# Optimization experiments

Hardware: AMD Instinct MI355X
Metric: run time of the kernel (lower is better)

The kernel has to match this reference:

```python
import jax, jax.numpy as jnp
import numpy as np


def _gcn_layer(x, W, b, src, dst, norm, n_nodes):
    # PyG GCNConv: h = x @ W, then degree-normalized scatter-add over edges (incl. self loops), then + bias
    h = x @ W                                   # [N, F_out]
    msg = h[src] * norm[:, None]                # [E+N, F_out]
    out = jax.ops.segment_sum(msg, dst, num_segments=n_nodes)
    return out + b


def _norm_and_loops(edge_index, n_nodes):
    # add self loops, compute symmetric normalization deg^-1/2[src]*deg^-1/2[dst]
    loop = jnp.arange(n_nodes, dtype=edge_index.dtype)
    src = jnp.concatenate([edge_index[0], loop])
    dst = jnp.concatenate([edge_index[1], loop])
    deg = jax.ops.segment_sum(jnp.ones_like(dst, dtype=jnp.float32), dst, num_segments=n_nodes)
    dinv = jnp.where(deg > 0, jax.lax.rsqrt(deg), 0.0)
    norm = dinv[src] * dinv[dst]
    return src, dst, norm


def setup_inputs() -> dict:
    key = jax.random.key(0)
    k1, k2, k3, k4 = jax.random.split(key, 4)
    N, E, F = 100000, 1600000, 512
    x = jax.random.normal(k1, (N, F), dtype=jnp.float32)
    edge_index = jax.random.randint(k2, (2, E), 0, N, dtype=jnp.int64)
    W1 = jax.random.normal(k3, (F, 128), dtype=jnp.float32) * (1.0 / np.sqrt(F))
    b1 = jnp.zeros((128,), dtype=jnp.float32)
    W2 = jax.random.normal(k4, (128, 64), dtype=jnp.float32) * (1.0 / np.sqrt(128))
    b2 = jnp.zeros((64,), dtype=jnp.float32)
    return {"x": x, "edge_index": edge_index, "W1": W1, "b1": b1, "W2": W2, "b2": b2}


def reference(x, edge_index, W1, b1, W2, b2):
    n_nodes = x.shape[0]
    src, dst, norm = _norm_and_loops(edge_index, n_nodes)
    h = jax.nn.relu(_gcn_layer(x, W1, b1, src, dst, norm, n_nodes))
    z = jax.nn.relu(_gcn_layer(h, W2, b2, src, dst, norm, n_nodes))
    return z
```

## Files before the change

### kernel.cpp

```cpp
#include <hip/hip_runtime.h>

#define SCAN_B 1024

using f16x8 = __attribute__((ext_vector_type(8))) _Float16;
using f32x4 = __attribute__((ext_vector_type(4))) float;
typedef _Float16 half4v __attribute__((ext_vector_type(4)));
typedef _Float16 half8v __attribute__((ext_vector_type(8)));


__global__ void zero2_kernel(int* __restrict__ a, int* __restrict__ b, int n) {
  int i = blockIdx.x * blockDim.x + threadIdx.x;
  if (i < n) { a[i] = 0; b[i] = 0; }
}

__global__ void count_kernel(const int* __restrict__ ei, int* __restrict__ cnt, int E) {
  int i = blockIdx.x * blockDim.x + threadIdx.x;
  if (i < E) atomicAdd(&cnt[ei[E + i]], 1);
}

__global__ void scan1_kernel(const int* __restrict__ cnt, int* __restrict__ rowstart,
                             int* __restrict__ bsum, float* __restrict__ dinv, int n) {
  __shared__ int sm[SCAN_B];
  const int t = threadIdx.x;
  const int i = blockIdx.x * SCAN_B + t;
  int c = (i < n) ? cnt[i] : 0;
  if (i < n) dinv[i] = rsqrtf((float)(c + 1));
  int v = (i < n) ? (c + 1) : 0;
  sm[t] = v;
  __syncthreads();
  for (int off = 1; off < SCAN_B; off <<= 1) {
    int x = (t >= off) ? sm[t - off] : 0;
    __syncthreads();
    if (t >= off) sm[t] += x;
    __syncthreads();
  }
  if (i < n) rowstart[i] = sm[t] - v;
  if (t == SCAN_B - 1) bsum[blockIdx.x] = sm[t];
}

__global__ void scan2_kernel(int* __restrict__ bsum, int nb) {
  __shared__ int sm[SCAN_B];
  const int t = threadIdx.x;
  int v = (t < nb) ? bsum[t] : 0;
  sm[t] = v;
  __syncthreads();
  for (int off = 1; off < SCAN_B; off <<= 1) {
    int x = (t >= off) ? sm[t - off] : 0;
    __syncthreads();
    if (t >= off) sm[t] += x;
    __syncthreads();
  }
  if (t < nb) bsum[t] = sm[t] - v;
}

__global__ void scan3_kernel(int* __restrict__ rowstart, const int* __restrict__ bsum, int n) {
  int i = blockIdx.x * blockDim.x + threadIdx.x;
  if (i < n) rowstart[i] += bsum[i / SCAN_B];
}

__global__ void fillself_kernel(const int* __restrict__ ei, int* __restrict__ fillc,
                                const int* __restrict__ rowstart, const int* __restrict__ cnt,
                                const float* __restrict__ dinv, float2* __restrict__ ew,
                                int E, int N) {
  int i = blockIdx.x * blockDim.x + threadIdx.x;
  if (i < E) {
    int s = ei[i];
    int d = ei[E + i];
    int p = atomicAdd(&fillc[d], 1);
    ew[rowstart[d] + p] = make_float2(__int_as_float(s), dinv[s] * dinv[d]);
  } else if (i < E + N) {
    int n = i - E;
    float dn = dinv[n];
    ew[rowstart[n] + cnt[n]] = make_float2(__int_as_float(n), dn * dn);
  }
}

__global__ void wconv2_kernel(const float* __restrict__ W1, _Float16* __restrict__ W1t, int K1, int N1,
                              const float* __restrict__ W2, _Float16* __restrict__ W2t, int K2, int N2) {
  int i = blockIdx.x * blockDim.x + threadIdx.x;
  const int n1 = K1 * N1;
  if (i < n1) {
    int k = i / N1, n = i % N1;
    W1t[(size_t)n * K1 + k] = (_Float16)W1[i];
  } else if (i < n1 + K2 * N2) {
    int j = i - n1;
    int k = j / N2, n = j % N2;
    W2t[(size_t)n * K2 + k] = (_Float16)W2[j];
  }
}


template <int BM, int BN, typename AT, typename CT>
__global__ void __launch_bounds__(512, 2)
gemm_mfma_kernel(const AT* __restrict__ A, const _Float16* __restrict__ Wt,
                 CT* __restrict__ C, int M, int K) {
  constexpr int BK   = 32;
  constexpr int LDK  = 40;
  constexpr int MR   = BM / 2 / 16;
  constexpr int NR   = BN / 4 / 16;
  constexpr int N    = BN;
  constexpr int LDC  = NR * 16 + 4;
  constexpr int SMA  = (BM + BN) * LDK * 2;
  constexpr int SME  = 8 * 16 * LDC * 4;
  constexpr int SMEM = SMA > SME ? SMA : SME;

  __shared__ __align__(16) char smem[SMEM];
  _Float16* Asm = (_Float16*)smem;
  _Float16* Bsm = Asm + (size_t)BM * LDK;

  const int tid  = threadIdx.x;
  const int lane = tid & 63;
  const int w    = tid >> 6;
  const int wm   = w >> 2;
  const int wn   = w & 3;
  const int fr   = lane & 15;
  const int fq   = lane >> 4;
  const int m0   = blockIdx.x * BM;

  constexpr bool A32 = sizeof(AT) == 4;
  const int a_c = A32 ? (tid & 7) : (tid & 3);
  const int a_m = A32 ? (tid >> 3) : (tid >> 2);
  const int br  = tid >> 2;
  const int bj  = tid & 3;

  float4 av32[2];
  uint4  av16;
  uint4  bt;

  auto loadA = [&](int kt) {
    if constexpr (A32) {
#pragma unroll
      for (int p = 0; p < 2; ++p) {
        const int gm = m0 + a_m + 64 * p;
        av32[p] = (gm < M) ? *(const float4*)&A[(size_t)gm * K + kt + 4 * a_c]
                           : make_float4(0.f, 0.f, 0.f, 0.f);
      }
    } else {
      const int gm = m0 + a_m;
      av16 = (gm < M) ? *(const uint4*)&A[(size_t)gm * K + kt + 8 * a_c]
                      : make_uint4(0u, 0u, 0u, 0u);
    }
  };
  auto loadB = [&](int kt) {
    if (tid < BN * 4) bt = *(const uint4*)&Wt[(size_t)br * K + kt + 8 * bj];
  };

  f32x4 acc[MR][NR] = {};

  loadA(0);
  loadB(0);

  for (int kt = 0; kt < K; kt += BK) {
    __syncthreads();

    if constexpr (A32) {
#pragma unroll
      for (int p = 0; p < 2; ++p) {
        const int r = a_m + 64 * p;
        half4v hv = {(_Float16)av32[p].x, (_Float16)av32[p].y,
                     (_Float16)av32[p].z, (_Float16)av32[p].w};
        *(half4v*)((char*)Asm + r * (LDK * 2) + a_c * 8) = hv;
      }
    } else {
      *(uint4*)((char*)Asm + a_m * (LDK * 2) + a_c * 16) = av16;
    }
    if (tid < BN * 4) *(uint4*)((char*)Bsm + br * (LDK * 2) + 16 * bj) = bt;
    __syncthreads();

    if (kt + BK < K) {
      loadA(kt + BK);
      loadB(kt + BK);
    }

    f16x8 bfrag[NR];
#pragma unroll
    for (int ni = 0; ni < NR; ++ni) {
      const int r = wn * (NR * 16) + ni * 16 + fr;
      bfrag[ni] = *(const f16x8*)((const char*)Bsm + r * (LDK * 2) + fq * 16);
    }
#pragma unroll
    for (int mi = 0; mi < MR; ++mi) {
      const int r = wm * 64 + mi * 16 + fr;
      f16x8 afrag = *(const f16x8*)((const char*)Asm + r * (LDK * 2) + fq * 16);
#pragma unroll
      for (int ni = 0; ni < NR; ++ni)
        acc[mi][ni] = __builtin_amdgcn_mfma_f32_16x16x32_f16(afrag, bfrag[ni], acc[mi][ni], 0, 0, 0);
    }
  }

  __syncthreads();
  {
    float* cst = (float*)smem + (size_t)w * (16 * LDC);
    constexpr int CPR   = NR * 4;
    constexpr int EPASS = (16 * CPR + 63) / 64;
#pragma unroll
    for (int mi = 0; mi < MR; ++mi) {
#pragma unroll
      for (int ni = 0; ni < NR; ++ni)
#pragma unroll
        for (int r = 0; r < 4; ++r)
          cst[(fq * 4 + r) * LDC + ni * 16 + fr] = acc[mi][ni][r];
#pragma unroll
      for (int p = 0; p < EPASS; ++p) {
        const int idx = p * 64 + lane;
        if (idx < 16 * CPR) {
          const int row = idx / CPR;
          const int ch  = idx % CPR;
          const int gm  = m0 + wm * 64 + mi * 16 + row;
          float4 v = *(const float4*)&cst[row * LDC + ch * 4];
          if (gm < M) {
            if constexpr (sizeof(CT) == 2) {
              half4v hv = {(_Float16)v.x, (_Float16)v.y, (_Float16)v.z, (_Float16)v.w};
              *(half4v*)&C[(size_t)gm * N + wn * (NR * 16) + ch * 4] = hv;
            } else {
              *(float4*)&C[(size_t)gm * N + wn * (NR * 16) + ch * 4] = v;
            }
          }
        }
      }
    }
  }
}


template <int F, typename OT>
__global__ void agg_kernel(const _Float16* __restrict__ hin, const int* __restrict__ rowstart,
                           const int* __restrict__ cnt, const float2* __restrict__ ew,
                           const float* __restrict__ bias, OT* __restrict__ outp, int N) {
  constexpr int LPE = F / 8;
  constexpr int EPW = 64 / LPE;
  const int wave = (int)((blockIdx.x * (size_t)blockDim.x + threadIdx.x) >> 6);
  if (wave >= N) return;
  const int lane = threadIdx.x & 63;
  const int sub  = lane / LPE;
  const int c    = lane % LPE;
  const int n    = wave;

  const int beg = rowstart[n];
  const int end = beg + cnt[n] + 1;

  float acc[8] = {};
  int j = beg + sub;
  for (; j + 3 * EPW < end; j += 4 * EPW) {
    const float2 e0 = ew[j];
    const float2 e1 = ew[j + EPW];
    const float2 e2 = ew[j + 2 * EPW];
    const float2 e3 = ew[j + 3 * EPW];
    const half8v v0 = *(const half8v*)&hin[(size_t)__float_as_int(e0.x) * F + c * 8];
    const half8v v1 = *(const half8v*)&hin[(size_t)__float_as_int(e1.x) * F + c * 8];
    const half8v v2 = *(const half8v*)&hin[(size_t)__float_as_int(e2.x) * F + c * 8];
    const half8v v3 = *(const half8v*)&hin[(size_t)__float_as_int(e3.x) * F + c * 8];
#pragma unroll
    for (int i = 0; i < 8; ++i) {
      acc[i] = fmaf((float)v0[i], e0.y, acc[i]);
      acc[i] = fmaf((float)v1[i], e1.y, acc[i]);
      acc[i] = fmaf((float)v2[i], e2.y, acc[i]);
      acc[i] = fmaf((float)v3[i], e3.y, acc[i]);
    }
  }
  for (; j < end; j += EPW) {
    const float2 e = ew[j];
    const half8v v = *(const half8v*)&hin[(size_t)__float_as_int(e.x) * F + c * 8];
#pragma unroll
    for (int i = 0; i < 8; ++i) acc[i] = fmaf((float)v[i], e.y, acc[i]);
  }

#pragma unroll
  for (int d = LPE; d < 64; d <<= 1)
#pragma unroll
    for (int i = 0; i < 8; ++i) acc[i] += __shfl_xor(acc[i], d);

  if (lane < LPE) {
    const float4 b0 = *(const float4*)&bias[c * 8];
    const float4 b1 = *(const float4*)&bias[c * 8 + 4];
    float r[8];
    r[0] = fmaxf(acc[0] + b0.x, 0.f);
    r[1] = fmaxf(acc[1] + b0.y, 0.f);
    r[2] = fmaxf(acc[2] + b0.z, 0.f);
    r[3] = fmaxf(acc[3] + b0.w, 0.f);
    r[4] = fmaxf(acc[4] + b1.x, 0.f);
    r[5] = fmaxf(acc[5] + b1.y, 0.f);
    r[6] = fmaxf(acc[6] + b1.z, 0.f);
    r[7] = fmaxf(acc[7] + b1.w, 0.f);
    if constexpr (sizeof(OT) == 2) {
      half8v hv;
#pragma unroll
      for (int i = 0; i < 8; ++i) hv[i] = (_Float16)r[i];
      *(half8v*)&outp[(size_t)n * F + c * 8] = hv;
    } else {
      *(float4*)&outp[(size_t)n * F + c * 8]     = make_float4(r[0], r[1], r[2], r[3]);
      *(float4*)&outp[(size_t)n * F + c * 8 + 4] = make_float4(r[4], r[5], r[6], r[7]);
    }
  }
}


extern "C" void kernel_launch(void* const* d_in, const int* in_sizes, int n_in,
                              void* d_out, int out_size, void* d_ws, size_t ws_size,
                              hipStream_t stream) {
  const float* x  = (const float*)d_in[0];
  const int*   ei = (const int*)d_in[1];
  const float* W1 = (const float*)d_in[2];
  const float* b1 = (const float*)d_in[3];
  const float* W2 = (const float*)d_in[4];
  const float* b2 = (const float*)d_in[5];
  float* out = (float*)d_out;

  const int F1 = in_sizes[3];
  const int F2 = in_sizes[5];
  const int F0 = in_sizes[2] / F1;
  const int N  = in_sizes[0] / F0;
  const int E  = in_sizes[1] / 2;

  char* ws = (char*)d_ws;
  size_t off = 0;
  auto alloc = [&](size_t bytes) -> void* {
    void* p = ws + off;
    off = (off + bytes + 255) & ~(size_t)255;
    return p;
  };

  int*    cnt      = (int*)alloc((size_t)N * 4);
  int*    fillc    = (int*)alloc((size_t)N * 4);
  int*    rowstart = (int*)alloc((size_t)N * 4);
  float*  dinv     = (float*)alloc((size_t)N * 4);
  const int nb     = (N + SCAN_B - 1) / SCAN_B;
  int*    bsum     = (int*)alloc((size_t)nb * 4);
  float2* ew       = (float2*)alloc(((size_t)E + N) * 8);
  _Float16* h      = (_Float16*)alloc((size_t)N * F1 * 2);
  _Float16* h1     = (_Float16*)alloc((size_t)N * F1 * 2);
  _Float16* h2     = h;
  _Float16* W1t    = (_Float16*)alloc((size_t)F0 * F1 * 2);
  _Float16* W2t    = (_Float16*)alloc((size_t)F1 * F2 * 2);

  zero2_kernel<<<(N + 255) / 256, 256, 0, stream>>>(cnt, fillc, N);
  count_kernel<<<(E + 255) / 256, 256, 0, stream>>>(ei, cnt, E);
  scan1_kernel<<<nb, SCAN_B, 0, stream>>>(cnt, rowstart, bsum, dinv, N);
  scan2_kernel<<<1, SCAN_B, 0, stream>>>(bsum, nb);
  scan3_kernel<<<(N + 255) / 256, 256, 0, stream>>>(rowstart, bsum, N);
  fillself_kernel<<<(E + N + 255) / 256, 256, 0, stream>>>(ei, fillc, rowstart, cnt, dinv, ew, E, N);
  wconv2_kernel<<<(F0 * F1 + F1 * F2 + 255) / 256, 256, 0, stream>>>(
      W1, W1t, F0, F1, W2, W2t, F1, F2);

  gemm_mfma_kernel<128, 128, float, _Float16><<<(N + 127) / 128, 512, 0, stream>>>(x, W1t, h, N, F0);
  {
    const long blocks = ((long)N * 64 + 255) / 256;
    agg_kernel<128, _Float16><<<(int)blocks, 256, 0, stream>>>(h, rowstart, cnt, ew, b1, h1, N);
  }

  gemm_mfma_kernel<128, 64, _Float16, _Float16><<<(N + 127) / 128, 512, 0, stream>>>(h1, W2t, h2, N, F1);
  {
    const long blocks = ((long)N * 64 + 255) / 256;
    agg_kernel<64, float><<<(int)blocks, 256, 0, stream>>>(h2, rowstart, cnt, ew, b2, out, N);
  }
}
```

Measured before the change: 349.5 us.

## Replace three-kernel scan with single-pass chained scan and fold weight conversion into init

```diff
diff --git a/kernel.cpp b/kernel.cpp
--- a/kernel.cpp
+++ b/kernel.cpp
@@ -8,9 +8,24 @@
 typedef _Float16 half8v __attribute__((ext_vector_type(8)));
 
 
-__global__ void zero2_kernel(int* __restrict__ a, int* __restrict__ b, int n) {
+__global__ void init_kernel(int* __restrict__ cnt, int* __restrict__ fillc,
+                            int* __restrict__ partial, int* __restrict__ ticket,
+                            int N, int nb,
+                            const float* __restrict__ W1, _Float16* __restrict__ W1t, int K1, int N1,
+                            const float* __restrict__ W2, _Float16* __restrict__ W2t, int K2, int N2) {
   int i = blockIdx.x * blockDim.x + threadIdx.x;
-  if (i < n) { a[i] = 0; b[i] = 0; }
+  if (i < N) { cnt[i] = 0; fillc[i] = 0; }
+  if (i < nb) partial[i] = -1;
+  if (i == 0) *ticket = 0;
+  const int n1 = K1 * N1;
+  if (i < n1) {
+    int k = i / N1, n = i % N1;
+    W1t[(size_t)n * K1 + k] = (_Float16)W1[i];
+  } else if (i < n1 + K2 * N2) {
+    int j = i - n1;
+    int k = j / N2, n = j % N2;
+    W2t[(size_t)n * K2 + k] = (_Float16)W2[j];
+  }
 }
 
 __global__ void count_kernel(const int* __restrict__ ei, int* __restrict__ cnt, int E) {
@@ -18,11 +33,17 @@
   if (i < E) atomicAdd(&cnt[ei[E + i]], 1);
 }
 
-__global__ void scan1_kernel(const int* __restrict__ cnt, int* __restrict__ rowstart,
-                             int* __restrict__ bsum, float* __restrict__ dinv, int n) {
+__global__ void scan_onepass_kernel(const int* __restrict__ cnt, int* __restrict__ rowstart,
+                                    float* __restrict__ dinv, int* __restrict__ ticket,
+                                    int* __restrict__ partial, int n) {
   __shared__ int sm[SCAN_B];
+  __shared__ int s_bid, s_prefix;
   const int t = threadIdx.x;
-  const int i = blockIdx.x * SCAN_B + t;
+  if (t == 0) s_bid = atomicAdd(ticket, 1);
+  __syncthreads();
+  const int bid = s_bid;
+  const int i = bid * SCAN_B + t;
+
   int c = (i < n) ? cnt[i] : 0;
   if (i < n) dinv[i] = rsqrtf((float)(c + 1));
   int v = (i < n) ? (c + 1) : 0;
@@ -34,28 +55,22 @@
     if (t >= off) sm[t] += x;
     __syncthreads();
   }
-  if (i < n) rowstart[i] = sm[t] - v;
-  if (t == SCAN_B - 1) bsum[blockIdx.x] = sm[t];
-}
-
-__global__ void scan2_kernel(int* __restrict__ bsum, int nb) {
-  __shared__ int sm[SCAN_B];
-  const int t = threadIdx.x;
-  int v = (t < nb) ? bsum[t] : 0;
-  sm[t] = v;
+
+  if (t == 0) {
+    int prefix = 0;
+    if (bid > 0) {
+      int p;
+      do {
+        p = __hip_atomic_load(&partial[bid - 1], __ATOMIC_ACQUIRE, __HIP_MEMORY_SCOPE_AGENT);
+      } while (p < 0);
+      prefix = p;
+    }
+    __hip_atomic_store(&partial[bid], prefix + sm[SCAN_B - 1],
+                       __ATOMIC_RELEASE, __HIP_MEMORY_SCOPE_AGENT);
+    s_prefix = prefix;
+  }
   __syncthreads();
-  for (int off = 1; off < SCAN_B; off <<= 1) {
-    int x = (t >= off) ? sm[t - off] : 0;
-    __syncthreads();
-    if (t >= off) sm[t] += x;
-    __syncthreads();
-  }
-  if (t < nb) bsum[t] = sm[t] - v;
-}
-
-__global__ void scan3_kernel(int* __restrict__ rowstart, const int* __restrict__ bsum, int n) {
-  int i = blockIdx.x * blockDim.x + threadIdx.x;
-  if (i < n) rowstart[i] += bsum[i / SCAN_B];
+  if (i < n) rowstart[i] = s_prefix + sm[t] - v;
 }
 
 __global__ void fillself_kernel(const int* __restrict__ ei, int* __restrict__ fillc,
@@ -72,20 +87,6 @@
     int n = i - E;
     float dn = dinv[n];
     ew[rowstart[n] + cnt[n]] = make_float2(__int_as_float(n), dn * dn);
-  }
-}
-
-__global__ void wconv2_kernel(const float* __restrict__ W1, _Float16* __restrict__ W1t, int K1, int N1,
-                              const float* __restrict__ W2, _Float16* __restrict__ W2t, int K2, int N2) {
-  int i = blockIdx.x * blockDim.x + threadIdx.x;
-  const int n1 = K1 * N1;
-  if (i < n1) {
-    int k = i / N1, n = i % N1;
-    W1t[(size_t)n * K1 + k] = (_Float16)W1[i];
-  } else if (i < n1 + K2 * N2) {
-    int j = i - n1;
-    int k = j / N2, n = j % N2;
-    W2t[(size_t)n * K2 + k] = (_Float16)W2[j];
   }
 }
 
@@ -325,7 +326,8 @@
   int*    rowstart = (int*)alloc((size_t)N * 4);
   float*  dinv     = (float*)alloc((size_t)N * 4);
   const int nb     = (N + SCAN_B - 1) / SCAN_B;
-  int*    bsum     = (int*)alloc((size_t)nb * 4);
+  int*    partial  = (int*)alloc((size_t)nb * 4);
+  int*    ticket   = (int*)alloc(256);
   float2* ew       = (float2*)alloc(((size_t)E + N) * 8);
   _Float16* h      = (_Float16*)alloc((size_t)N * F1 * 2);
   _Float16* h1     = (_Float16*)alloc((size_t)N * F1 * 2);
@@ -333,14 +335,11 @@
   _Float16* W1t    = (_Float16*)alloc((size_t)F0 * F1 * 2);
   _Float16* W2t    = (_Float16*)alloc((size_t)F1 * F2 * 2);
 
-  zero2_kernel<<<(N + 255) / 256, 256, 0, stream>>>(cnt, fillc, N);
+  init_kernel<<<(N + 255) / 256, 256, 0, stream>>>(cnt, fillc, partial, ticket, N, nb,
+                                                   W1, W1t, F0, F1, W2, W2t, F1, F2);
   count_kernel<<<(E + 255) / 256, 256, 0, stream>>>(ei, cnt, E);
-  scan1_kernel<<<nb, SCAN_B, 0, stream>>>(cnt, rowstart, bsum, dinv, N);
-  scan2_kernel<<<1, SCAN_B, 0, stream>>>(bsum, nb);
-  scan3_kernel<<<(N + 255) / 256, 256, 0, stream>>>(rowstart, bsum, N);
+  scan_onepass_kernel<<<nb, SCAN_B, 0, stream>>>(cnt, rowstart, dinv, ticket, partial, N);
   fillself_kernel<<<(E + N + 255) / 256, 256, 0, stream>>>(ei, fillc, rowstart, cnt, dinv, ew, E, N);
-  wconv2_kernel<<<(F0 * F1 + F1 * F2 + 255) / 256, 256, 0, stream>>>(
-      W1, W1t, F0, F1, W2, W2t, F1, F2);
 
   gemm_mfma_kernel<128, 128, float, _Float16><<<(N + 127) / 128, 512, 0, stream>>>(x, W1t, h, N, F0);
   {
```

New measurement: 485.4 us. 1.39x slower.
